# Kernel tuning notes

Measured on AMD Instinct MI355X. Metric: run time of the kernel, lower is better.

## Reference

```python
import jax, jax.numpy as jnp
import numpy as np

B, S, E, NH = 1, 2048, 1024, 8
DH = E // NH
EPS = 1e-6


def setup_inputs() -> dict:
    key = jax.random.key(0)
    ks = jax.random.split(key, 7)
    q = jax.random.normal(ks[0], (B, S, E), dtype=jnp.float32)
    k = jax.random.normal(ks[1], (B, S, E), dtype=jnp.float32)
    v = jax.random.normal(ks[2], (B, S, E), dtype=jnp.float32)
    # gate projections (original inits kernel=0; use small random to keep math non-degenerate)
    Wi = jax.random.normal(ks[3], (3 * E, NH), dtype=jnp.float32) * 0.02
    bi = jax.random.normal(ks[4], (NH,), dtype=jnp.float32) * 0.1
    Wf = jax.random.normal(ks[5], (3 * E, NH), dtype=jnp.float32) * 0.02
    bf = jnp.linspace(3.0, 6.0, NH, dtype=jnp.float32)  # bias_linspace_initializer(3,6)
    ln_scale = jnp.ones((E,), dtype=jnp.float32)
    return {"q": q, "k": k, "v": v, "Wi": Wi, "bi": bi, "Wf": Wf, "bf": bf, "ln_scale": ln_scale}


def _mlstm_forward(q, k, v, Wi, bi, Wf, bf, ln_scale):
    # gate preactivations: (B, NH, S, 1)
    gate_in = jnp.concatenate([q, k, v], axis=-1)  # (B, S, 3E)
    i_pre = jnp.transpose(gate_in @ Wi + bi, (0, 2, 1))[..., None]
    f_pre = jnp.transpose(gate_in @ Wf + bf, (0, 2, 1))[..., None]

    # heads: (B, NH, S, DH)
    qh = jnp.transpose(q.reshape(B, S, NH, DH), (0, 2, 1, 3))
    kh = jnp.transpose(k.reshape(B, S, NH, DH), (0, 2, 1, 3))
    vh = jnp.transpose(v.reshape(B, S, NH, DH), (0, 2, 1, 3))

    # cumulative log forget gates -> decay matrix fm[i,j] = sum_{t=j+1..i} log_sigmoid(f_t)
    log_fg = jax.nn.log_sigmoid(f_pre)                  # (B, NH, S, 1)
    cum = jnp.cumsum(log_fg, axis=2)[..., 0]            # (B, NH, S)
    fm = cum[:, :, :, None] - cum[:, :, None, :]        # (B, NH, S, S)

    mask = jnp.tril(jnp.ones((S, S), dtype=bool))
    log_D = jnp.where(mask, fm + i_pre[..., 0][:, :, None, :], -jnp.inf)  # + igate of column j

    max_log_D = jnp.max(log_D, axis=-1, keepdims=True)  # row-wise stabilizer (B, NH, S, 1)
    D = jnp.exp(log_D - max_log_D)

    qk = jnp.einsum("bhsd,bhtd->bhst", qh, kh) / jnp.sqrt(jnp.float32(DH))
    C = qk * D
    normalizer = jnp.maximum(jnp.abs(C.sum(axis=-1, keepdims=True)), jnp.exp(-max_log_D))
    h = jnp.einsum("bhst,bhtd->bhsd", C / (normalizer + EPS), vh)  # (B, NH, S, DH)

    # per-head layernorm over DH, scale of size E reshaped per head, no bias
    mu = h.mean(axis=-1, keepdims=True)
    var = h.var(axis=-1, keepdims=True)
    h_norm = (h - mu) * jax.lax.rsqrt(var + EPS) * ln_scale.reshape(1, NH, 1, DH)

    return jnp.transpose(h_norm, (0, 2, 1, 3)).reshape(B, S, E)


def reference(q, k, v, Wi, bi, Wf, bf, ln_scale):
    return _mlstm_forward(q, k, v, Wi, bi, Wf, bf, ln_scale)
```

## Files before the change

kernel.cpp:

```cpp
#include <hip/hip_runtime.h>
#include <math.h>

namespace {
constexpr int S  = 2048;
constexpr int E  = 1024;
constexpr int NH = 8;
constexpr int DH = 128;
constexpr float EPSF = 1e-6f;
constexpr float INV_LN2 = 1.4426950408889634f;
}

typedef short short8 __attribute__((ext_vector_type(8)));
typedef float f32x16 __attribute__((ext_vector_type(16)));
typedef float f32x4  __attribute__((ext_vector_type(4)));

__device__ __forceinline__ unsigned short f2bf(float x) {
  unsigned int u = __float_as_uint(x);
  unsigned int r = (u + 0x7fffu + ((u >> 16) & 1u)) >> 16;
  return (unsigned short)r;
}

__device__ __forceinline__ void async_copy16(const void* g, void* l) {
  __builtin_amdgcn_global_load_lds(
      (const __attribute__((address_space(1))) unsigned int*)g,
      (__attribute__((address_space(3))) unsigned int*)l, 16, 0, 0);
}

__global__ __launch_bounds__(256) void merged_pre_kernel(
    const float* __restrict__ q, const float* __restrict__ k, const float* __restrict__ v,
    const float* __restrict__ Wi, const float* __restrict__ Wf,
    const float* __restrict__ bi, const float* __restrict__ bfg,
    unsigned short* __restrict__ qb, unsigned short* __restrict__ kb,
    unsigned short* __restrict__ vt,
    float* __restrict__ ipre, float* __restrict__ lsf)
{
  __shared__ __align__(16) char smem[38912];
  const int b = blockIdx.x;
  const int tid = threadIdx.x;

  if (b < 128) {
    const int wv = tid >> 6, lane = tid & 63;
    const int m0 = b * 16;
    const int tr = lane & 15;
    const int ks = (lane >> 4) * 8;
    unsigned short* Wl = (unsigned short*)smem + wv * (16*264);
    float* red = (float*)(smem + 33792);
    f32x4 acc = {0.f, 0.f, 0.f, 0.f};
    const float* srcs[3] = {q, k, v};
    #pragma unroll
    for (int p = 0; p < 3; ++p) {
      const size_t wb = ((size_t)p*E + wv*256) * 8;
      #pragma unroll
      for (int it = 0; it < 8; ++it) {
        const int f = it*64 + lane;
        float4 wi4 = *reinterpret_cast<const float4*>(Wi + wb + (size_t)f*4);
        float4 wf4 = *reinterpret_cast<const float4*>(Wf + wb + (size_t)f*4);
        const int el = f >> 1, n0 = (f & 1) * 4;
        Wl[(n0+0)*264 + el] = f2bf(wi4.x);
        Wl[(n0+1)*264 + el] = f2bf(wi4.y);
        Wl[(n0+2)*264 + el] = f2bf(wi4.z);
        Wl[(n0+3)*264 + el] = f2bf(wi4.w);
        Wl[(n0+8)*264 + el] = f2bf(wf4.x);
        Wl[(n0+9)*264 + el] = f2bf(wf4.y);
        Wl[(n0+10)*264 + el] = f2bf(wf4.z);
        Wl[(n0+11)*264 + el] = f2bf(wf4.w);
      }
      const float* src = srcs[p];
      #pragma unroll
      for (int s = 0; s < 8; ++s) {
        const float* ap = src + (size_t)(m0 + tr)*E + wv*256 + s*32 + ks;
        float4 a0 = *reinterpret_cast<const float4*>(ap);
        float4 a1 = *reinterpret_cast<const float4*>(ap + 4);
        short8 af;
        af[0] = (short)f2bf(a0.x); af[1] = (short)f2bf(a0.y);
        af[2] = (short)f2bf(a0.z); af[3] = (short)f2bf(a0.w);
        af[4] = (short)f2bf(a1.x); af[5] = (short)f2bf(a1.y);
        af[6] = (short)f2bf(a1.z); af[7] = (short)f2bf(a1.w);
        short8 bf8 = *reinterpret_cast<const short8*>(&Wl[tr*264 + s*32 + ks]);
        acc = __builtin_amdgcn_mfma_f32_16x16x32_bf16(af, bf8, acc, 0, 0, 0);
      }
    }
    #pragma unroll
    for (int r = 0; r < 4; ++r)
      red[wv*256 + (lane&15)*16 + (lane>>4)*4 + r] = acc[r];
    __syncthreads();
    {
      const int n = tid & 15, m = tid >> 4;
      float val = red[0*256 + n*16 + m] + red[1*256 + n*16 + m]
                + red[2*256 + n*16 + m] + red[3*256 + n*16 + m];
      const int t = m0 + m;
      if (n < 8) {
        ipre[n*S + t] = val + bi[n];
      } else {
        float fp = val + bfg[n-8];
        lsf[(n-8)*S + t] = fminf(fp, 0.f) - log1pf(__expf(-fabsf(fp)));
      }
    }
  } else if (b < 640) {
    float (*Ts)[65] = (float(*)[65])smem;
    const int bb = b - 128;
    const int j0 = (bb & 31) * 64;
    const int d0 = ((bb >> 5) & 1) * 64;
    const int h  = bb >> 6;
    const int c = tid & 63, r4 = tid >> 6;
    #pragma unroll
    for (int rr = 0; rr < 16; ++rr) {
      int r = r4*16 + rr;
      Ts[r][c] = v[(size_t)(j0 + r)*E + h*DH + d0 + c];
    }
    __syncthreads();
    #pragma unroll
    for (int rr = 0; rr < 16; ++rr) {
      int r = r4*16 + rr;
      vt[(size_t)(h*DH + d0 + r)*S + j0 + c] = f2bf(Ts[c][r]);
    }
  } else {
    const int bb = b - 640;
    constexpr int N4 = S*E/4;
    const float4* src = (bb < 256) ? (const float4*)q : (const float4*)k;
    ushort4* dst = (bb < 256) ? (ushort4*)qb : (ushort4*)kb;
    const int b0 = (bb & 255);
    for (int i = b0*256 + tid; i < N4; i += 256*256) {
      float4 x = src[i];
      ushort4 o;
      o.x = f2bf(x.x); o.y = f2bf(x.y); o.z = f2bf(x.z); o.w = f2bf(x.w);
      dst[i] = o;
    }
  }
}

__global__ __launch_bounds__(256) void scan_kernel(
    const float* __restrict__ ipre, const float* __restrict__ lsf,
    float* __restrict__ a2_out, float* __restrict__ m2_out)
{
  const int h = blockIdx.x, tid = threadIdx.x;
  const int lane = tid & 63, wv = tid >> 6;
  constexpr int PER = S / 256;
  const int base = h*S + tid*PER;
  __shared__ float wred[4], wmax[4];

  float c[PER];
  float run = 0.f;
  #pragma unroll
  for (int u = 0; u < PER; u++) { run += lsf[base+u]; c[u] = run; }
  float s = run;
  #pragma unroll
  for (int off = 1; off < 64; off <<= 1) {
    float t = __shfl_up(s, off);
    if (lane >= off) s += t;
  }
  if (lane == 63) wred[wv] = s;
  __syncthreads();
  float wpre = 0.f;
  for (int i = 0; i < wv; i++) wpre += wred[i];
  const float excl = wpre + (s - run);

  float av[PER], mloc[PER];
  float lm = -INFINITY;
  #pragma unroll
  for (int u = 0; u < PER; u++) {
    c[u] += excl;
    av[u] = ipre[base+u] - c[u];
    lm = fmaxf(lm, av[u]);
    mloc[u] = lm;
  }
  float sm_ = lm;
  #pragma unroll
  for (int off = 1; off < 64; off <<= 1) {
    float t = __shfl_up(sm_, off);
    if (lane >= off) sm_ = fmaxf(sm_, t);
  }
  if (lane == 63) wmax[wv] = sm_;
  __syncthreads();
  float wpm = -INFINITY;
  for (int i = 0; i < wv; i++) wpm = fmaxf(wpm, wmax[i]);
  float prev = __shfl_up(sm_, 1);
  if (lane == 0) prev = -INFINITY;
  const float exclm = fmaxf(wpm, prev);
  #pragma unroll
  for (int u = 0; u < PER; u++) {
    float m = fmaxf(exclm, mloc[u]);
    a2_out[base+u] = av[u] * INV_LN2;
    m2_out[base+u] = m * INV_LN2;
  }
}

__global__ __launch_bounds__(256, 2) void attn_kernel(
    const unsigned short* __restrict__ qb, const unsigned short* __restrict__ kb,
    const unsigned short* __restrict__ vt,
    const float* __restrict__ a2g, const float* __restrict__ m2g,
    const float* __restrict__ ln, float* __restrict__ opart,
    float* __restrict__ out)
{
  const int h   = blockIdx.x & 7;
  const int idx = blockIdx.x >> 3;
  int qt, part, nspl;
  if (idx < 56)      { qt = 63 - (idx >> 1);        part = idx & 1; nspl = 2; }
  else if (idx < 64) { qt = 31 - (idx - 56);        part = 0;       nspl = 1; }
  else if (idx < 72) { qt = 35 - ((idx - 64) >> 1); part = idx & 1; nspl = 2; }
  else               { qt = 23 - (idx - 72);        part = 0;       nspl = 1; }
  const int N = (qt + 4) >> 2;
  const int jt_lo = part ? (N >> 1) : 0;
  const int jt_hi = (nspl == 2 && part == 0) ? (N >> 1) : N;

  const int tid = threadIdx.x;
  const int w = tid >> 6, lane = tid & 63, l31 = lane & 31, half = lane >> 5;
  const int qi0 = qt * 32;
  const int jcol_off = 32*w + l31;

  __shared__ short Klds[128*128];
  __shared__ short Vlds[128*128];
  __shared__ short Psm[32*136];
  __shared__ float mrow[32];
  float* Hs = (float*)Klds;

  if (tid < 32) mrow[tid] = m2g[h*S + qi0 + tid];

  short8 qf[8];
  #pragma unroll
  for (int s = 0; s < 8; ++s)
    qf[s] = *reinterpret_cast<const short8*>(
        qb + (size_t)(qi0 + l31)*E + h*DH + 16*s + 8*half);

  __syncthreads();
  float mreg[16];
  #pragma unroll
  for (int r = 0; r < 16; ++r) mreg[r] = mrow[(r&3) + 8*(r>>2) + 4*half];

  f32x16 acc = {0,0,0,0,0,0,0,0,0,0,0,0,0,0,0,0};

  const int lrow4 = lane >> 4;
  const int jb    = lane & 15;
  const int kq_row = 32*w + l31;
  const int kq_swz = kq_row & 15;

  for (int jt = jt_lo; jt < jt_hi; ++jt) {
    const int j0 = jt * 128;
    __syncthreads();
    #pragma unroll
    for (int i = 0; i < 8; ++i) {
      const int ii  = w*8 + i;
      const int row = ii*4 + lrow4;
      const int cc  = jb ^ (row & 15);
      async_copy16(kb + (size_t)(j0 + row)*E + h*DH + cc*8, &Klds[ii*512]);
      async_copy16(vt + (size_t)(h*DH + row)*S + j0 + cc*8, &Vlds[ii*512]);
    }
    const float ajv = a2g[h*S + j0 + jcol_off];
    __syncthreads();

    f32x16 qk = {0,0,0,0,0,0,0,0,0,0,0,0,0,0,0,0};
    #pragma unroll
    for (int s = 0; s < 8; ++s) {
      short8 kf = *reinterpret_cast<const short8*>(
          &Klds[kq_row*128 + ((2*s + half) ^ kq_swz) * 8]);
      qk = __builtin_amdgcn_mfma_f32_32x32x16_bf16(qf[s], kf, qk, 0, 0, 0);
    }
    const int jcol = j0 + jcol_off;
    #pragma unroll
    for (int r = 0; r < 16; ++r) {
      const int iloc = (r&3) + 8*(r>>2) + 4*half;
      float pv = (jcol <= qi0 + iloc) ? qk[r] * exp2f(ajv - mreg[r]) : 0.f;
      Psm[iloc*136 + jcol_off] = (short)f2bf(pv);
    }
    __syncthreads();
    #pragma unroll
    for (int s = 0; s < 8; ++s) {
      short8 pf = *reinterpret_cast<const short8*>(&Psm[l31*136 + 16*s + 8*half]);
      short8 vf = *reinterpret_cast<const short8*>(
          &Vlds[kq_row*128 + ((2*s + half) ^ kq_swz) * 8]);
      acc = __builtin_amdgcn_mfma_f32_32x32x16_bf16(pf, vf, acc, 0, 0, 0);
    }
  }

  if (nspl == 2) {
    const int pairid = (qt - 32)*8 + h;
    float* dst = opart + ((size_t)pairid*2 + part)*(32*128);
    #pragma unroll
    for (int r = 0; r < 16; ++r) {
      const int iloc = (r&3) + 8*(r>>2) + 4*half;
      dst[iloc*128 + 32*w + l31] = acc[r];
    }
    return;
  }

  __syncthreads();
  #pragma unroll
  for (int r = 0; r < 16; ++r)
    Hs[((r&3) + 8*(r>>2) + 4*half)*132 + 32*w + l31] = acc[r];
  __syncthreads();
  {
    const int row = tid >> 3, seg = tid & 7;
    float vals[16];
    #pragma unroll
    for (int c4 = 0; c4 < 4; ++c4) {
      float4 v4 = *reinterpret_cast<const float4*>(&Hs[row*132 + seg*16 + c4*4]);
      vals[c4*4+0]=v4.x; vals[c4*4+1]=v4.y; vals[c4*4+2]=v4.z; vals[c4*4+3]=v4.w;
    }
    float s1 = 0.f, s2 = 0.f;
    #pragma unroll
    for (int c = 0; c < 16; ++c) { s1 += vals[c]; s2 = fmaf(vals[c], vals[c], s2); }
    #pragma unroll
    for (int off = 1; off < 8; off <<= 1) {
      s1 += __shfl_xor(s1, off);
      s2 += __shfl_xor(s2, off);
    }
    const float mu = s1 * (1.f/128.f);
    float var = fmaxf(s2 * (1.f/128.f) - mu*mu, 0.f);
    const float rs = rsqrtf(var + EPSF);
    const size_t ob = (size_t)(qi0 + row)*E + h*DH + seg*16;
    #pragma unroll
    for (int c = 0; c < 16; ++c)
      out[ob + c] = (vals[c] - mu) * rs * ln[h*DH + seg*16 + c];
  }
}

__global__ __launch_bounds__(256) void combine_kernel(
    const float* __restrict__ opart, const float* __restrict__ ln,
    float* __restrict__ out)
{
  const int t = blockIdx.x;
  const int qt = 32 + (t >> 3);
  const int h  = t & 7;
  const float* p0 = opart + (size_t)((qt - 32)*8 + h)*2*(32*128);
  const float* p1 = p0 + 32*128;
  const int tid = threadIdx.x;
  const int row = tid >> 3, seg = tid & 7;
  float vals[16];
  #pragma unroll
  for (int c4 = 0; c4 < 4; ++c4) {
    float4 a = *reinterpret_cast<const float4*>(&p0[row*128 + seg*16 + c4*4]);
    float4 b = *reinterpret_cast<const float4*>(&p1[row*128 + seg*16 + c4*4]);
    vals[c4*4+0] = a.x + b.x; vals[c4*4+1] = a.y + b.y;
    vals[c4*4+2] = a.z + b.z; vals[c4*4+3] = a.w + b.w;
  }
  float s1 = 0.f, s2 = 0.f;
  #pragma unroll
  for (int c = 0; c < 16; ++c) { s1 += vals[c]; s2 = fmaf(vals[c], vals[c], s2); }
  #pragma unroll
  for (int off = 1; off < 8; off <<= 1) {
    s1 += __shfl_xor(s1, off);
    s2 += __shfl_xor(s2, off);
  }
  const float mu = s1 * (1.f/128.f);
  float var = fmaxf(s2 * (1.f/128.f) - mu*mu, 0.f);
  const float rs = rsqrtf(var + EPSF);
  const size_t ob = (size_t)(qt*32 + row)*E + h*DH + seg*16;
  #pragma unroll
  for (int c = 0; c < 16; ++c)
    out[ob + c] = (vals[c] - mu) * rs * ln[h*DH + seg*16 + c];
}

extern "C" void kernel_launch(void* const* d_in, const int* in_sizes, int n_in,
                              void* d_out, int out_size, void* d_ws, size_t ws_size,
                              hipStream_t stream) {
  const float* q  = (const float*)d_in[0];
  const float* k  = (const float*)d_in[1];
  const float* v  = (const float*)d_in[2];
  const float* Wi = (const float*)d_in[3];
  const float* bi = (const float*)d_in[4];
  const float* Wf = (const float*)d_in[5];
  const float* bf = (const float*)d_in[6];
  const float* ln = (const float*)d_in[7];
  float* out = (float*)d_out;

  char* base = (char*)d_ws;
  unsigned short* qb  = (unsigned short*)(base);
  unsigned short* kb  = (unsigned short*)(base + (size_t)S*E*2);
  unsigned short* vt  = (unsigned short*)(base + (size_t)S*E*4);
  float* fbase = (float*)(base + (size_t)S*E*6);
  float* ipre  = fbase;
  float* lsf   = fbase + 1*NH*S;
  float* a2    = fbase + 2*NH*S;
  float* m2    = fbase + 3*NH*S;
  float* opart = fbase + 4*NH*S;

  merged_pre_kernel<<<dim3(1152), dim3(256), 0, stream>>>(
      q, k, v, Wi, Wf, bi, bf, qb, kb, vt, ipre, lsf);
  scan_kernel<<<dim3(NH), dim3(256), 0, stream>>>(ipre, lsf, a2, m2);
  attn_kernel<<<dim3(768), dim3(256), 0, stream>>>(qb, kb, vt, a2, m2, ln, opart, out);
  combine_kernel<<<dim3(256), dim3(256), 0, stream>>>(opart, ln, out);
}
```

Measured before the change: 129.5 us.

## Use 64-wide key tiles and table-driven up-to-4-way split-K attention scheduling

Shrinks the key tile from 128 to 64 columns, which cuts LDS use and allows three blocks per CU. A lookup table orders jobs longest-first and splits long query tiles into up to four key-range parts instead of two. The grid grows to 1280 blocks and the combine kernel now sums a variable number of partials. The cost is that only two of four waves do the QK MFMA per tile, there are twice as many barriers per key range, and the partial buffer traffic is larger.

New measurement: 133.3 us. 3.0% more time.

```diff
diff --git a/kernel.cpp b/kernel.cpp
--- a/kernel.cpp
+++ b/kernel.cpp
@@ -25,6 +25,35 @@
       (const __attribute__((address_space(1))) unsigned int*)g,
       (__attribute__((address_space(3))) unsigned int*)l, 16, 0, 0);
 }
+
+__device__ const unsigned char JOB_QT[160] = {
+  63,63,63,63, 62,62,62,62, 61,61,61,61, 60,60,60,60,
+  59,59,59,59, 58,58,58,58, 57,57,57,57, 56,56,56,56,
+  47,47,47, 46,46,46, 45,45,45, 44,44,44, 43,43,43, 42,42,42,
+  31,31, 30,30, 29,29, 28,28, 15, 14,
+  55,55,55,55, 54,54,54,54, 53,53,53,53, 52,52,52,52,
+  51,51,51,51, 50,50,50,50, 49,49,49,49, 48,48,48,48,
+  41,41,41, 40,40,40, 39,39,39, 38,38,38, 37,37,37, 36,36,36,
+  27,27, 26,26, 25,25, 24,24, 13, 12,
+  35,35,35, 34,34,34, 33,33,33, 32,32,32,
+  23,23, 22,22, 21,21, 20,20, 11, 10,
+  19,19, 18,18, 17,17, 16,16, 9, 8,
+  7, 6, 5, 4, 3, 2, 1, 0
+};
+__device__ const unsigned char JOB_PART[160] = {
+  0,1,2,3, 0,1,2,3, 0,1,2,3, 0,1,2,3,
+  0,1,2,3, 0,1,2,3, 0,1,2,3, 0,1,2,3,
+  0,1,2, 0,1,2, 0,1,2, 0,1,2, 0,1,2, 0,1,2,
+  0,1, 0,1, 0,1, 0,1, 0, 0,
+  0,1,2,3, 0,1,2,3, 0,1,2,3, 0,1,2,3,
+  0,1,2,3, 0,1,2,3, 0,1,2,3, 0,1,2,3,
+  0,1,2, 0,1,2, 0,1,2, 0,1,2, 0,1,2, 0,1,2,
+  0,1, 0,1, 0,1, 0,1, 0, 0,
+  0,1,2, 0,1,2, 0,1,2, 0,1,2,
+  0,1, 0,1, 0,1, 0,1, 0, 0,
+  0,1, 0,1, 0,1, 0,1, 0, 0,
+  0, 0, 0, 0, 0, 0, 0, 0
+};
 
 __global__ __launch_bounds__(256) void merged_pre_kernel(
     const float* __restrict__ q, const float* __restrict__ k, const float* __restrict__ v,
@@ -185,7 +214,7 @@
   }
 }
 
-__global__ __launch_bounds__(256, 2) void attn_kernel(
+__global__ __launch_bounds__(256, 3) void attn_kernel(
     const unsigned short* __restrict__ qb, const unsigned short* __restrict__ kb,
     const unsigned short* __restrict__ vt,
     const float* __restrict__ a2g, const float* __restrict__ m2g,
@@ -194,23 +223,20 @@
 {
   const int h   = blockIdx.x & 7;
   const int idx = blockIdx.x >> 3;
-  int qt, part, nspl;
-  if (idx < 56)      { qt = 63 - (idx >> 1);        part = idx & 1; nspl = 2; }
-  else if (idx < 64) { qt = 31 - (idx - 56);        part = 0;       nspl = 1; }
-  else if (idx < 72) { qt = 35 - ((idx - 64) >> 1); part = idx & 1; nspl = 2; }
-  else               { qt = 23 - (idx - 72);        part = 0;       nspl = 1; }
-  const int N = (qt + 4) >> 2;
-  const int jt_lo = part ? (N >> 1) : 0;
-  const int jt_hi = (nspl == 2 && part == 0) ? (N >> 1) : N;
+  const int qt   = JOB_QT[idx];
+  const int part = JOB_PART[idx];
+  const int kparts = 1 + (qt >> 4);
+  const int N = (qt + 2) >> 1;
+  const int jt_lo = (N * part) / kparts;
+  const int jt_hi = (N * (part + 1)) / kparts;
 
   const int tid = threadIdx.x;
   const int w = tid >> 6, lane = tid & 63, l31 = lane & 31, half = lane >> 5;
   const int qi0 = qt * 32;
-  const int jcol_off = 32*w + l31;
-
-  __shared__ short Klds[128*128];
-  __shared__ short Vlds[128*128];
-  __shared__ short Psm[32*136];
+
+  __shared__ short Klds[64*128];
+  __shared__ short Vlds[128*64];
+  __shared__ short Psm[32*72];
   __shared__ float mrow[32];
   float* Hs = (float*)Klds;
 
@@ -229,56 +255,63 @@
 
   f32x16 acc = {0,0,0,0,0,0,0,0,0,0,0,0,0,0,0,0};
 
+  const int jb    = lane & 15;
   const int lrow4 = lane >> 4;
-  const int jb    = lane & 15;
-  const int kq_row = 32*w + l31;
-  const int kq_swz = kq_row & 15;
+  const int vrow8 = lane >> 3;
+  const int vb7   = lane & 7;
+  const int jq    = 32*w + l31;
 
   for (int jt = jt_lo; jt < jt_hi; ++jt) {
-    const int j0 = jt * 128;
+    const int j0 = jt * 64;
     __syncthreads();
     #pragma unroll
-    for (int i = 0; i < 8; ++i) {
-      const int ii  = w*8 + i;
-      const int row = ii*4 + lrow4;
-      const int cc  = jb ^ (row & 15);
-      async_copy16(kb + (size_t)(j0 + row)*E + h*DH + cc*8, &Klds[ii*512]);
-      async_copy16(vt + (size_t)(h*DH + row)*S + j0 + cc*8, &Vlds[ii*512]);
-    }
-    const float ajv = a2g[h*S + j0 + jcol_off];
+    for (int i = 0; i < 4; ++i) {
+      const int ii  = w*4 + i;
+      const int kr  = ii*4 + lrow4;
+      const int kcc = jb ^ (kr & 15);
+      async_copy16(kb + (size_t)(j0 + kr)*E + h*DH + kcc*8, &Klds[ii*512]);
+      const int vr  = ii*8 + vrow8;
+      const int vcc = vb7 ^ (vr & 7);
+      async_copy16(vt + (size_t)(h*DH + vr)*S + j0 + vcc*8, &Vlds[ii*512]);
+    }
+    float ajv = 0.f;
+    if (w < 2) ajv = a2g[h*S + j0 + jq];
     __syncthreads();
 
-    f32x16 qk = {0,0,0,0,0,0,0,0,0,0,0,0,0,0,0,0};
-    #pragma unroll
-    for (int s = 0; s < 8; ++s) {
-      short8 kf = *reinterpret_cast<const short8*>(
-          &Klds[kq_row*128 + ((2*s + half) ^ kq_swz) * 8]);
-      qk = __builtin_amdgcn_mfma_f32_32x32x16_bf16(qf[s], kf, qk, 0, 0, 0);
-    }
-    const int jcol = j0 + jcol_off;
+    if (w < 2) {
+      f32x16 qk = {0,0,0,0,0,0,0,0,0,0,0,0,0,0,0,0};
+      #pragma unroll
+      for (int s = 0; s < 8; ++s) {
+        short8 kf = *reinterpret_cast<const short8*>(
+            &Klds[jq*128 + ((2*s + half) ^ (jq & 15)) * 8]);
+        qk = __builtin_amdgcn_mfma_f32_32x32x16_bf16(qf[s], kf, qk, 0, 0, 0);
+      }
+      const int jcol = j0 + jq;
+      #pragma unroll
+      for (int r = 0; r < 16; ++r) {
+        const int iloc = (r&3) + 8*(r>>2) + 4*half;
+        float pv = (jcol <= qi0 + iloc) ? qk[r] * exp2f(ajv - mreg[r]) : 0.f;
+        Psm[iloc*72 + jq] = (short)f2bf(pv);
+      }
+    }
+    __syncthreads();
+
+    #pragma unroll
+    for (int s = 0; s < 4; ++s) {
+      short8 pf = *reinterpret_cast<const short8*>(&Psm[l31*72 + 16*s + 8*half]);
+      short8 vf = *reinterpret_cast<const short8*>(
+          &Vlds[jq*64 + ((2*s + half) ^ (jq & 7)) * 8]);
+      acc = __builtin_amdgcn_mfma_f32_32x32x16_bf16(pf, vf, acc, 0, 0, 0);
+    }
+  }
+
+  if (kparts >= 2) {
+    const int pairid = (qt - 16)*8 + h;
+    float* dst = opart + ((size_t)pairid*4 + part)*(32*128);
     #pragma unroll
     for (int r = 0; r < 16; ++r) {
       const int iloc = (r&3) + 8*(r>>2) + 4*half;
-      float pv = (jcol <= qi0 + iloc) ? qk[r] * exp2f(ajv - mreg[r]) : 0.f;
-      Psm[iloc*136 + jcol_off] = (short)f2bf(pv);
-    }
-    __syncthreads();
-    #pragma unroll
-    for (int s = 0; s < 8; ++s) {
-      short8 pf = *reinterpret_cast<const short8*>(&Psm[l31*136 + 16*s + 8*half]);
-      short8 vf = *reinterpret_cast<const short8*>(
-          &Vlds[kq_row*128 + ((2*s + half) ^ kq_swz) * 8]);
-      acc = __builtin_amdgcn_mfma_f32_32x32x16_bf16(pf, vf, acc, 0, 0, 0);
-    }
-  }
-
-  if (nspl == 2) {
-    const int pairid = (qt - 32)*8 + h;
-    float* dst = opart + ((size_t)pairid*2 + part)*(32*128);
-    #pragma unroll
-    for (int r = 0; r < 16; ++r) {
-      const int iloc = (r&3) + 8*(r>>2) + 4*half;
-      dst[iloc*128 + 32*w + l31] = acc[r];
+      dst[iloc*128 + jq] = acc[r];
     }
     return;
   }
@@ -286,14 +319,14 @@
   __syncthreads();
   #pragma unroll
   for (int r = 0; r < 16; ++r)
-    Hs[((r&3) + 8*(r>>2) + 4*half)*132 + 32*w + l31] = acc[r];
+    Hs[((r&3) + 8*(r>>2) + 4*half)*128 + jq] = acc[r];
   __syncthreads();
   {
     const int row = tid >> 3, seg = tid & 7;
     float vals[16];
     #pragma unroll
     for (int c4 = 0; c4 < 4; ++c4) {
-      float4 v4 = *reinterpret_cast<const float4*>(&Hs[row*132 + seg*16 + c4*4]);
+      float4 v4 = *reinterpret_cast<const float4*>(&Hs[row*128 + seg*16 + c4*4]);
       vals[c4*4+0]=v4.x; vals[c4*4+1]=v4.y; vals[c4*4+2]=v4.z; vals[c4*4+3]=v4.w;
     }
     float s1 = 0.f, s2 = 0.f;
@@ -319,19 +352,27 @@
     float* __restrict__ out)
 {
   const int t = blockIdx.x;
-  const int qt = 32 + (t >> 3);
+  const int qt = 16 + (t >> 3);
   const int h  = t & 7;
-  const float* p0 = opart + (size_t)((qt - 32)*8 + h)*2*(32*128);
-  const float* p1 = p0 + 32*128;
+  const int kparts = 1 + (qt >> 4);
+  const float* p0 = opart + (size_t)((qt - 16)*8 + h)*4*(32*128);
   const int tid = threadIdx.x;
   const int row = tid >> 3, seg = tid & 7;
   float vals[16];
   #pragma unroll
   for (int c4 = 0; c4 < 4; ++c4) {
     float4 a = *reinterpret_cast<const float4*>(&p0[row*128 + seg*16 + c4*4]);
-    float4 b = *reinterpret_cast<const float4*>(&p1[row*128 + seg*16 + c4*4]);
-    vals[c4*4+0] = a.x + b.x; vals[c4*4+1] = a.y + b.y;
-    vals[c4*4+2] = a.z + b.z; vals[c4*4+3] = a.w + b.w;
+    vals[c4*4+0] = a.x; vals[c4*4+1] = a.y;
+    vals[c4*4+2] = a.z; vals[c4*4+3] = a.w;
+  }
+  for (int p = 1; p < kparts; ++p) {
+    const float* pp = p0 + (size_t)p*(32*128);
+    #pragma unroll
+    for (int c4 = 0; c4 < 4; ++c4) {
+      float4 a = *reinterpret_cast<const float4*>(&pp[row*128 + seg*16 + c4*4]);
+      vals[c4*4+0] += a.x; vals[c4*4+1] += a.y;
+      vals[c4*4+2] += a.z; vals[c4*4+3] += a.w;
+    }
   }
   float s1 = 0.f, s2 = 0.f;
   #pragma unroll
@@ -377,6 +418,6 @@
   merged_pre_kernel<<<dim3(1152), dim3(256), 0, stream>>>(
       q, k, v, Wi, Wf, bi, bf, qb, kb, vt, ipre, lsf);
   scan_kernel<<<dim3(NH), dim3(256), 0, stream>>>(ipre, lsf, a2, m2);
-  attn_kernel<<<dim3(768), dim3(256), 0, stream>>>(qb, kb, vt, a2, m2, ln, opart, out);
-  combine_kernel<<<dim3(256), dim3(256), 0, stream>>>(opart, ln, out);
-}
+  attn_kernel<<<dim3(1280), dim3(256), 0, stream>>>(qb, kb, vt, a2, m2, ln, opart, out);
+  combine_kernel<<<dim3(384), dim3(256), 0, stream>>>(opart, ln, out);
+}
```
